# Kernel tuning notes

Measured on AMD Instinct MI355X. Metric: run time of the kernel, lower is better.

Reference implementation:

```python
import jax, jax.numpy as jnp
import numpy as np

B, N, D, E = 256, 192, 512, 1024
H = E // 2          # MLP hidden = 512
K = 58              # round(0.3 * 192), hardcoded in the torch forward
EPS_L2 = 1e-8
EPS_BN = 1e-5


def setup_inputs() -> dict:
    key = jax.random.key(0)
    ks = jax.random.split(key, 8)
    s = 0.02
    return {
        "all_patch_embeddings": jax.random.normal(ks[0], (B, N, D), dtype=jnp.float32),
        "attention_map": jax.random.uniform(ks[1], (B, N + 1, N + 1), dtype=jnp.float32),
        # fc: Linear(D, E)
        "W_fc": jax.random.normal(ks[2], (E, D), dtype=jnp.float32) * s,
        "b_fc": jnp.zeros((E,), dtype=jnp.float32),
        # mlp layer 0: Linear(D, H) + BatchNorm1d(H) + ReLU
        "W1": jax.random.normal(ks[3], (H, D), dtype=jnp.float32) * s,
        "b1": jnp.zeros((H,), dtype=jnp.float32),
        "gamma1": jnp.ones((H,), dtype=jnp.float32),
        "beta1": jnp.zeros((H,), dtype=jnp.float32),
        # mlp layer 1: Linear(H, E) (no BN/ReLU applied on last layer)
        "W2": jax.random.normal(ks[4], (E, H), dtype=jnp.float32) * s,
        "b2": jnp.zeros((E,), dtype=jnp.float32),
    }


def reference(all_patch_embeddings, attention_map, W_fc, b_fc, W1, b1, gamma1, beta1, W2, b2):
    # CLS-row attention over the 192 patch tokens: [B, N]
    cls_attn = attention_map[:, 0, 1:]
    # torch.sort(descending)[...,:K] == top-k indices (batched, replaces python loop)
    _, idx = jax.lax.top_k(cls_attn, K)                      # [B, K] int32
    # batched gather replacing the per-sample index_select loop
    sel = jnp.take_along_axis(all_patch_embeddings, idx[:, :, None], axis=1)  # [B, K, D]
    # l2norm over last dim
    norm = jnp.sqrt(jnp.sum(sel * sel, axis=-1, keepdims=True)) + EPS_L2
    base = sel / norm
    # .half() cast in the original (round-trip to fp16 precision)
    base = base.astype(jnp.float16).astype(jnp.float32)
    # fc branch
    feat_fc = jnp.einsum('bkd,ed->bke', base, W_fc) + b_fc    # [B, K, E]
    # mlp branch (num_layers=2): Linear -> BN(train-mode batch stats) -> ReLU -> Linear
    h = jnp.einsum('bkd,hd->bkh', base, W1) + b1              # [B, K, H]
    hf = h.reshape(B * K, H)
    mu = jnp.mean(hf, axis=0)
    var = jnp.var(hf, axis=0)
    hf = (hf - mu) * jax.lax.rsqrt(var + EPS_BN) * gamma1 + beta1
    h = jax.nn.relu(hf).reshape(B, K, H)
    feat_mlp = jnp.einsum('bkh,eh->bke', h, W2) + b2          # [B, K, E]
    feats = feat_mlp + feat_fc
    # maxk_pool1d_var with k=1 and lengths == K reduces to max over token dim
    return jnp.max(feats, axis=1).astype(jnp.float32)         # [B, E]
```

## Files before the change

### kernel.cpp

```cpp
#include <hip/hip_runtime.h>
#include <hip/hip_fp16.h>

#define B_ 256
#define N_ 192
#define D_ 512
#define E_ 1024
#define H_ 512
#define K_ 58
#define M_ (B_*K_)
#define M2_ (B_*64)

typedef _Float16 f16;
typedef unsigned int u32;
typedef _Float16 half8 __attribute__((ext_vector_type(8)));
typedef float floatx16 __attribute__((ext_vector_type(16)));

#define WAIT_VMCNT0() asm volatile("s_waitcnt vmcnt(0)" ::: "memory")
#define BAR()         __builtin_amdgcn_s_barrier()
#define PRIO1()       __builtin_amdgcn_s_setprio(1)
#define PRIO0()       __builtin_amdgcn_s_setprio(0)

__device__ inline half8 cvt8(float4 f0, float4 f1) {
  half8 r;
  r[0]=(f16)f0.x; r[1]=(f16)f0.y; r[2]=(f16)f0.z; r[3]=(f16)f0.w;
  r[4]=(f16)f1.x; r[5]=(f16)f1.y; r[6]=(f16)f1.z; r[7]=(f16)f1.w;
  return r;
}

__device__ inline void gl_lds16(const f16* g, f16* l) {
  __builtin_amdgcn_global_load_lds((const __attribute__((address_space(1))) u32*)g,
                                   (__attribute__((address_space(3))) u32*)l, 16, 0, 0);
}

__device__ inline void stage128(const f16* gbase, int gstride, f16* sT, int w, int lane) {
  int lrow  = lane >> 2;
  int chunk = (lane & 3) ^ ((lane >> 3) & 3);
  gl_lds16(gbase + (size_t)(w*16      + lrow)*gstride + chunk*8, &sT[(w*16)*32]);
  gl_lds16(gbase + (size_t)(64 + w*16 + lrow)*gstride + chunk*8, &sT[(64 + w*16)*32]);
}

__device__ inline void stage_half(const f16* gbase, f16* sT, int h, int w, int lane) {
  int lrow = lane >> 3;
  int cg   = (lane & 7) ^ lrow;
  int r0 = h*128 + w*16;
  gl_lds16(gbase + (size_t)(r0     + lrow)*1024 + cg*8, &sT[(size_t)r0*64]);
  gl_lds16(gbase + (size_t)(r0 + 8 + lrow)*1024 + cg*8, &sT[(size_t)(r0 + 8)*64]);
}

__global__ void setup_kernel(const float* __restrict__ Wfc, const float* __restrict__ W2,
                             const float* __restrict__ W1, const float* __restrict__ attn,
                             const float* __restrict__ emb,
                             f16* __restrict__ Wcat, f16* __restrict__ W1_16,
                             f16* __restrict__ A16, float* __restrict__ csum) {
  __shared__ float sv[N_];
  __shared__ int sidx[K_];
  __shared__ int cnt;
  int blk = blockIdx.x, t = threadIdx.x;
  if (blk < 512) {
    int idx = (blk*256 + t)*8;
    int e = idx >> 10, c = idx & 1023;
    const float* src = (c < 512) ? (Wfc + (size_t)e*512 + c)
                                 : (W2  + (size_t)e*512 + (c-512));
    half8 o = cvt8(((const float4*)src)[0], ((const float4*)src)[1]);
    *(uint4*)(Wcat + idx) = *(uint4*)&o;
  } else if (blk < 640) {
    int idx = ((blk-512)*256 + t)*8;
    const float* src = W1 + idx;
    half8 o = cvt8(((const float4*)src)[0], ((const float4*)src)[1]);
    *(uint4*)(W1_16 + idx) = *(uint4*)&o;
  } else if (blk < 896) {
    int b = blk - 640;
    if (t == 0) cnt = 0;
    if (t < N_) sv[t] = attn[(size_t)b*193*193 + 1 + t];
    __syncthreads();
    if (t < N_) {
      float v = sv[t]; int rank = 0;
      for (int j = 0; j < N_; ++j) {
        float vj = sv[j];
        rank += (vj > v) || (vj == v && j < t);
      }
      if (rank < K_) sidx[atomicAdd(&cnt, 1)] = t;
    }
    __syncthreads();
    int w = t >> 6, lane = t & 63;
    for (int slot = w; slot < 64; slot += 4) {
      f16* dst = A16 + ((size_t)b*64 + slot)*1024 + lane*8;
      if (slot < K_) {
        const float* src = emb + ((size_t)b*N_ + sidx[slot])*D_ + lane*8;
        float4 v0 = ((const float4*)src)[0];
        float4 v1 = ((const float4*)src)[1];
        float s = v0.x*v0.x + v0.y*v0.y + v0.z*v0.z + v0.w*v0.w
                + v1.x*v1.x + v1.y*v1.y + v1.z*v1.z + v1.w*v1.w;
        #pragma unroll
        for (int off = 32; off > 0; off >>= 1) s += __shfl_xor(s, off);
        float inv = 1.0f / (sqrtf(s) + 1e-8f);
        half8 o;
        o[0]=(f16)(v0.x*inv); o[1]=(f16)(v0.y*inv); o[2]=(f16)(v0.z*inv); o[3]=(f16)(v0.w*inv);
        o[4]=(f16)(v1.x*inv); o[5]=(f16)(v1.y*inv); o[6]=(f16)(v1.z*inv); o[7]=(f16)(v1.w*inv);
        *(uint4*)dst = *(uint4*)&o;
      } else {
        uint4 z; z.x=0u; z.y=0u; z.z=0u; z.w=0u;
        *(uint4*)dst = z;
      }
    }
  } else {
    float4 z; z.x=0.f; z.y=0.f; z.z=0.f; z.w=0.f;
    ((float4*)csum)[t] = z;
  }
}

__launch_bounds__(256, 2)
__global__ void gemm1_kernel(const f16* __restrict__ A16, const f16* __restrict__ W1_16,
                             const float* __restrict__ b1, f16* __restrict__ Aout,
                             float* __restrict__ csum, float* __restrict__ css) {
  __shared__ f16 sA[2][128*32];
  __shared__ f16 sB[2][128*32];
  __shared__ float sSum[4][64], sSS[4][64];
  int t = threadIdx.x;
  int g = blockIdx.x;
  int xcd = g & 7, rest = g >> 3;
  int n0 = (rest & 3) * 128;
  int m0 = (xcd + 8*(rest >> 2)) * 128;
  int lane = t & 63, w = t >> 6;
  int l31 = lane & 31, khalf = lane >> 5, swz = (l31 >> 1) & 3;
  int rw = w & 1, cw = w >> 1;
  floatx16 acc[2][2] = {};
  const f16* Ab = A16 + (size_t)m0*1024;
  const f16* Bb = W1_16 + (size_t)n0*512;
  stage128(Ab, 1024, sA[0], w, lane);
  stage128(Bb, 512,  sB[0], w, lane);
  __syncthreads();
  for (int it = 0; it < 16; ++it) {
    int cur = it & 1, nxt = cur ^ 1;
    if (it < 15) {
      stage128(Ab + (it+1)*32, 1024, sA[nxt], w, lane);
      stage128(Bb + (it+1)*32, 512,  sB[nxt], w, lane);
    }
    #pragma unroll
    for (int s = 0; s < 2; ++s) {
      int ko = ((s*2 + khalf) ^ swz) * 8;
      half8 a[2], bf[2];
      #pragma unroll
      for (int i = 0; i < 2; ++i) a[i]  = *(const half8*)&sA[cur][(rw*64 + i*32 + l31)*32 + ko];
      #pragma unroll
      for (int j = 0; j < 2; ++j) bf[j] = *(const half8*)&sB[cur][(cw*64 + j*32 + l31)*32 + ko];
      #pragma unroll
      for (int i = 0; i < 2; ++i)
        #pragma unroll
        for (int j = 0; j < 2; ++j)
          acc[i][j] = __builtin_amdgcn_mfma_f32_32x32x16_f16(a[i], bf[j], acc[i][j], 0, 0, 0);
    }
    __syncthreads();
  }
  #pragma unroll
  for (int jt = 0; jt < 2; ++jt) {
    int col = n0 + cw*64 + jt*32 + l31;
    float bias = b1[col];
    float s = 0.f, ss = 0.f;
    #pragma unroll
    for (int i = 0; i < 2; ++i) {
      #pragma unroll
      for (int rg = 0; rg < 16; ++rg) {
        int rib = i*32 + (rg&3) + 8*(rg>>2) + 4*khalf;
        float x = acc[i][jt][rg] + bias;
        Aout[(size_t)(m0 + rw*64 + rib)*1024 + 512 + col] = (f16)x;
        if (i == 0 || rib < K_) { s += x; ss += x*x; }
      }
    }
    s  += __shfl_xor(s, 32);
    ss += __shfl_xor(ss, 32);
    if (lane < 32) { sSum[w][jt*32 + l31] = s; sSS[w][jt*32 + l31] = ss; }
  }
  __syncthreads();
  if (t < 128) {
    int c = t;
    int w0 = 2*(c >> 6), ci = c & 63;
    atomicAdd(&csum[n0 + c], sSum[w0][ci] + sSum[w0+1][ci]);
    atomicAdd(&css[n0 + c],  sSS[w0][ci]  + sSS[w0+1][ci]);
  }
}

__global__ void bnrelu_kernel(f16* __restrict__ A, const float* __restrict__ csum,
                              const float* __restrict__ css, const float* __restrict__ gamma,
                              const float* __restrict__ beta) {
  int t = threadIdx.x, lane = t & 63, w = t >> 6;
  int col = lane * 8;
  float sc[8], sh[8];
  #pragma unroll
  for (int j = 0; j < 8; ++j) {
    int c = col + j;
    float mu  = csum[c] * (1.0f/M_);
    float var = css[c] * (1.0f/M_) - mu*mu;
    float s   = gamma[c] * rsqrtf(var + 1e-5f);
    sc[j] = s; sh[j] = beta[c] - mu*s;
  }
  int r0 = blockIdx.x * 16 + w;
  #pragma unroll
  for (int i = 0; i < 4; ++i) {
    f16* p = A + (size_t)(r0 + i*4)*1024 + 512 + col;
    uint4 u = *(const uint4*)p;
    half8 v = *(half8*)&u, o;
    #pragma unroll
    for (int j = 0; j < 8; ++j) o[j] = (f16)fmaxf((float)v[j]*sc[j] + sh[j], 0.f);
    *(uint4*)p = *(uint4*)&o;
  }
}

__launch_bounds__(512, 2)
__global__ void fused_kernel(const f16* __restrict__ A16, const f16* __restrict__ Wcat,
                             const float* __restrict__ bfc, const float* __restrict__ b2,
                             float* __restrict__ out) {
  __shared__ __align__(16) f16 sA[2][256*64];
  __shared__ __align__(16) f16 sB[2][256*64];
  __shared__ float sMax[4][256];
  int t = threadIdx.x;
  int g = blockIdx.x;
  int xcd = g & 7, rest = g >> 3;
  int nt = rest & 3;
  int bt = xcd + 8*(rest >> 2);
  int e0 = nt * 256;
  int lane = t & 63, w = t >> 6;
  int l31 = lane & 31, khalf = lane >> 5, swzr = l31 & 7;
  int wm = w >> 2, wn = w & 3;
  floatx16 acc[4][2] = {};
  const f16* Ab = A16 + (size_t)bt*256*1024;
  const f16* Bb = Wcat + (size_t)e0*1024;
  int aBase0 = (wm*128 +  0 + l31)*64;
  int aBase1 = (wm*128 + 32 + l31)*64;
  int aBase2 = (wm*128 + 64 + l31)*64;
  int aBase3 = (wm*128 + 96 + l31)*64;
  int bBase0 = (wn*64  +  0 + l31)*64;
  int bBase1 = (wn*64  + 32 + l31)*64;
  stage_half(Ab, sA[0], 0, w, lane);
  stage_half(Ab, sA[0], 1, w, lane);
  stage_half(Bb, sB[0], 0, w, lane);
  stage_half(Bb, sB[0], 1, w, lane);
  WAIT_VMCNT0(); BAR();
  int cur = 0;
  #pragma unroll 1
  for (int it = 0; it < 16; ++it) {
    int nxt = cur ^ 1;
    const f16* An = Ab + (it+1)*64;
    const f16* Bn = Bb + (it+1)*64;
    const f16* sAc = sA[cur];
    const f16* sBc = sB[cur];
    half8 a0f[4], a1f[4], a2f[4], a3f[4], b0v[4], b1v[4];
    #pragma unroll
    for (int s = 0; s < 4; ++s) {
      int ko = (((s<<1)|khalf) ^ swzr) << 3;
      a0f[s] = *(const half8*)&sAc[aBase0 + ko];
      a1f[s] = *(const half8*)&sAc[aBase1 + ko];
      b0v[s] = *(const half8*)&sBc[bBase0 + ko];
    }
    if (it < 15) stage_half(An, sA[nxt], 0, w, lane);
    BAR(); PRIO1();
    #pragma unroll
    for (int s = 0; s < 4; ++s) {
      acc[0][0] = __builtin_amdgcn_mfma_f32_32x32x16_f16(a0f[s], b0v[s], acc[0][0], 0,0,0);
      acc[1][0] = __builtin_amdgcn_mfma_f32_32x32x16_f16(a1f[s], b0v[s], acc[1][0], 0,0,0);
    }
    PRIO0(); BAR();
    #pragma unroll
    for (int s = 0; s < 4; ++s) {
      int ko = (((s<<1)|khalf) ^ swzr) << 3;
      b1v[s] = *(const half8*)&sBc[bBase1 + ko];
    }
    if (it < 15) stage_half(An, sA[nxt], 1, w, lane);
    BAR(); PRIO1();
    #pragma unroll
    for (int s = 0; s < 4; ++s) {
      acc[0][1] = __builtin_amdgcn_mfma_f32_32x32x16_f16(a0f[s], b1v[s], acc[0][1], 0,0,0);
      acc[1][1] = __builtin_amdgcn_mfma_f32_32x32x16_f16(a1f[s], b1v[s], acc[1][1], 0,0,0);
    }
    PRIO0(); BAR();
    #pragma unroll
    for (int s = 0; s < 4; ++s) {
      int ko = (((s<<1)|khalf) ^ swzr) << 3;
      a2f[s] = *(const half8*)&sAc[aBase2 + ko];
      a3f[s] = *(const half8*)&sAc[aBase3 + ko];
    }
    if (it < 15) stage_half(Bn, sB[nxt], 0, w, lane);
    BAR(); PRIO1();
    #pragma unroll
    for (int s = 0; s < 4; ++s) {
      acc[2][1] = __builtin_amdgcn_mfma_f32_32x32x16_f16(a2f[s], b1v[s], acc[2][1], 0,0,0);
      acc[3][1] = __builtin_amdgcn_mfma_f32_32x32x16_f16(a3f[s], b1v[s], acc[3][1], 0,0,0);
    }
    PRIO0(); BAR();
    if (it < 15) stage_half(Bn, sB[nxt], 1, w, lane);
    BAR(); PRIO1();
    #pragma unroll
    for (int s = 0; s < 4; ++s) {
      acc[2][0] = __builtin_amdgcn_mfma_f32_32x32x16_f16(a2f[s], b0v[s], acc[2][0], 0,0,0);
      acc[3][0] = __builtin_amdgcn_mfma_f32_32x32x16_f16(a3f[s], b0v[s], acc[3][0], 0,0,0);
    }
    PRIO0();
    WAIT_VMCNT0();
    BAR();
    cur = nxt;
  }
  #pragma unroll
  for (int p = 0; p < 2; ++p) {
    #pragma unroll
    for (int nf = 0; nf < 2; ++nf) {
      float mx = -3.0e38f;
      #pragma unroll
      for (int rg = 0; rg < 16; ++rg)
        mx = fmaxf(mx, acc[2*p][nf][rg]);
      #pragma unroll
      for (int rg = 0; rg < 16; ++rg) {
        int rowin = (rg&3) + 8*(rg>>2) + 4*khalf;
        if (rowin < K_ - 32) mx = fmaxf(mx, acc[2*p+1][nf][rg]);
      }
      mx = fmaxf(mx, __shfl_xor(mx, 32));
      if (lane < 32) sMax[wm*2 + p][wn*64 + nf*32 + l31] = mx;
    }
  }
  __syncthreads();
  #pragma unroll
  for (int j = 0; j < 2; ++j) {
    int idx = t + j*512;
    int bq = idx >> 8, c = idx & 255;
    int e = e0 + c;
    out[((size_t)bt*4 + bq)*E_ + e] = sMax[bq][c] + bfc[e] + b2[e];
  }
}

extern "C" void kernel_launch(void* const* d_in, const int* in_sizes, int n_in,
                              void* d_out, int out_size, void* d_ws, size_t ws_size,
                              hipStream_t stream) {
  const float* emb   = (const float*)d_in[0];
  const float* attn  = (const float*)d_in[1];
  const float* Wfc   = (const float*)d_in[2];
  const float* bfc   = (const float*)d_in[3];
  const float* W1    = (const float*)d_in[4];
  const float* b1    = (const float*)d_in[5];
  const float* gamma = (const float*)d_in[6];
  const float* beta  = (const float*)d_in[7];
  const float* W2    = (const float*)d_in[8];
  const float* b2    = (const float*)d_in[9];
  float* out = (float*)d_out;

  char* ws = (char*)d_ws;
  f16*   A16   = (f16*)(ws);
  f16*   Wcat  = (f16*)(ws + 33554432);
  f16*   W1_16 = (f16*)(ws + 35651584);
  float* csum  = (float*)(ws + 36175872);
  float* css   = (float*)(ws + 36177920);

  setup_kernel<<<897, 256, 0, stream>>>(Wfc, W2, W1, attn, emb, Wcat, W1_16, A16, csum);
  gemm1_kernel<<<512, 256, 0, stream>>>(A16, W1_16, b1, A16, csum, css);
  bnrelu_kernel<<<1024, 256, 0, stream>>>(A16, csum, css, gamma, beta);
  fused_kernel<<<256, 512, 0, stream>>>(A16, Wcat, bfc, b2, out);
}
```

Baseline: 236.6 us.

## Fuse BN+ReLU into GEMM1 via cooperative grid sync, rebalance fused-kernel staging

```diff
diff --git a/kernel.cpp b/kernel.cpp
--- a/kernel.cpp
+++ b/kernel.cpp
@@ -1,5 +1,8 @@
 #include <hip/hip_runtime.h>
 #include <hip/hip_fp16.h>
+#include <hip/hip_cooperative_groups.h>
+
+namespace cg = cooperative_groups;
 
 #define B_ 256
 #define N_ 192
@@ -112,7 +115,8 @@
 __launch_bounds__(256, 2)
 __global__ void gemm1_kernel(const f16* __restrict__ A16, const f16* __restrict__ W1_16,
                              const float* __restrict__ b1, f16* __restrict__ Aout,
-                             float* __restrict__ csum, float* __restrict__ css) {
+                             float* __restrict__ csum, float* __restrict__ css,
+                             const float* __restrict__ gamma, const float* __restrict__ beta) {
   __shared__ f16 sA[2][128*32];
   __shared__ f16 sB[2][128*32];
   __shared__ float sSum[4][64], sSS[4][64];
@@ -163,7 +167,6 @@
       for (int rg = 0; rg < 16; ++rg) {
         int rib = i*32 + (rg&3) + 8*(rg>>2) + 4*khalf;
         float x = acc[i][jt][rg] + bias;
-        Aout[(size_t)(m0 + rw*64 + rib)*1024 + 512 + col] = (f16)x;
         if (i == 0 || rib < K_) { s += x; ss += x*x; }
       }
     }
@@ -178,31 +181,26 @@
     atomicAdd(&csum[n0 + c], sSum[w0][ci] + sSum[w0+1][ci]);
     atomicAdd(&css[n0 + c],  sSS[w0][ci]  + sSS[w0+1][ci]);
   }
-}
-
-__global__ void bnrelu_kernel(f16* __restrict__ A, const float* __restrict__ csum,
-                              const float* __restrict__ css, const float* __restrict__ gamma,
-                              const float* __restrict__ beta) {
-  int t = threadIdx.x, lane = t & 63, w = t >> 6;
-  int col = lane * 8;
-  float sc[8], sh[8];
+  cg::this_grid().sync();
   #pragma unroll
-  for (int j = 0; j < 8; ++j) {
-    int c = col + j;
-    float mu  = csum[c] * (1.0f/M_);
-    float var = css[c] * (1.0f/M_) - mu*mu;
-    float s   = gamma[c] * rsqrtf(var + 1e-5f);
-    sc[j] = s; sh[j] = beta[c] - mu*s;
-  }
-  int r0 = blockIdx.x * 16 + w;
-  #pragma unroll
-  for (int i = 0; i < 4; ++i) {
-    f16* p = A + (size_t)(r0 + i*4)*1024 + 512 + col;
-    uint4 u = *(const uint4*)p;
-    half8 v = *(half8*)&u, o;
-    #pragma unroll
-    for (int j = 0; j < 8; ++j) o[j] = (f16)fmaxf((float)v[j]*sc[j] + sh[j], 0.f);
-    *(uint4*)p = *(uint4*)&o;
+  for (int jt = 0; jt < 2; ++jt) {
+    int col = n0 + cw*64 + jt*32 + l31;
+    float bias = b1[col];
+    float mu  = csum[col] * (1.0f/M_);
+    float var = css[col] * (1.0f/M_) - mu*mu;
+    float sc  = gamma[col] * rsqrtf(var + 1e-5f);
+    float sh  = beta[col] - mu*sc;
+    #pragma unroll
+    for (int i = 0; i < 2; ++i) {
+      #pragma unroll
+      for (int rg = 0; rg < 16; ++rg) {
+        int rib = i*32 + (rg&3) + 8*(rg>>2) + 4*khalf;
+        float x = acc[i][jt][rg] + bias;
+        float y = fmaxf(x*sc + sh, 0.f);
+        if (!(i == 0 || rib < K_)) y = 0.f;
+        Aout[(size_t)(m0 + rw*64 + rib)*1024 + 512 + col] = (f16)y;
+      }
+    }
   }
 }
 
@@ -265,7 +263,10 @@
       int ko = (((s<<1)|khalf) ^ swzr) << 3;
       b1v[s] = *(const half8*)&sBc[bBase1 + ko];
     }
-    if (it < 15) stage_half(An, sA[nxt], 1, w, lane);
+    if (it < 15) {
+      stage_half(An, sA[nxt], 1, w, lane);
+      stage_half(Bn, sB[nxt], 0, w, lane);
+    }
     BAR(); PRIO1();
     #pragma unroll
     for (int s = 0; s < 4; ++s) {
@@ -279,7 +280,7 @@
       a2f[s] = *(const half8*)&sAc[aBase2 + ko];
       a3f[s] = *(const half8*)&sAc[aBase3 + ko];
     }
-    if (it < 15) stage_half(Bn, sB[nxt], 0, w, lane);
+    if (it < 15) stage_half(Bn, sB[nxt], 1, w, lane);
     BAR(); PRIO1();
     #pragma unroll
     for (int s = 0; s < 4; ++s) {
@@ -287,7 +288,6 @@
       acc[3][1] = __builtin_amdgcn_mfma_f32_32x32x16_f16(a3f[s], b1v[s], acc[3][1], 0,0,0);
     }
     PRIO0(); BAR();
-    if (it < 15) stage_half(Bn, sB[nxt], 1, w, lane);
     BAR(); PRIO1();
     #pragma unroll
     for (int s = 0; s < 4; ++s) {
@@ -349,7 +349,18 @@
   float* css   = (float*)(ws + 36177920);
 
   setup_kernel<<<897, 256, 0, stream>>>(Wfc, W2, W1, attn, emb, Wcat, W1_16, A16, csum);
-  gemm1_kernel<<<512, 256, 0, stream>>>(A16, W1_16, b1, A16, csum, css);
-  bnrelu_kernel<<<1024, 256, 0, stream>>>(A16, csum, css, gamma, beta);
+
+  const f16* A16c = A16;
+  const f16* W1c  = W1_16;
+  f16* A16o = A16;
+  float* csumv = csum; float* cssv = css;
+  const float* b1c = b1; const float* gammac = gamma; const float* betac = beta;
+  void* gargs[8];
+  gargs[0] = (void*)&A16c;  gargs[1] = (void*)&W1c;   gargs[2] = (void*)&b1c;
+  gargs[3] = (void*)&A16o;  gargs[4] = (void*)&csumv; gargs[5] = (void*)&cssv;
+  gargs[6] = (void*)&gammac; gargs[7] = (void*)&betac;
+  hipLaunchCooperativeKernel((const void*)gemm1_kernel, dim3(512), dim3(256),
+                             gargs, 0, stream);
+
   fused_kernel<<<256, 512, 0, stream>>>(A16, Wcat, bfc, b2, out);
 }
```

Measured after the change: 305.1 us. 1.29x slower.
